# Performance work log

Measured on AMD Instinct MI355X. Metric: run time of the kernel, lower is better.

Reference implementation:

```python
import jax, jax.numpy as jnp
import numpy as np

B, N, G = 32, 262144, 256


def setup_inputs() -> dict:
    key = jax.random.key(0)
    k1, k2, k3 = jax.random.split(key, 3)
    pr = jax.random.normal(k1, (B, N), dtype=jnp.float32)
    inp_means = jax.random.normal(k2, (B, G), dtype=jnp.float32)
    vr = jax.random.randint(k3, (B, N, 1), 0, G, dtype=jnp.int32)
    W = jnp.ones((2,), dtype=jnp.float32)  # hist_weight, ones initializer
    return {"pr": pr, "inp_means": inp_means, "vr": vr, "W": W}


def reference(pr, inp_means, vr, W):
    sg = jax.lax.stop_gradient
    G = inp_means.shape[1]
    v = jnp.squeeze(vr, -1)  # [B, N] int cluster ids (stop_gradient in orig; int anyway)
    p_sg = sg(pr)

    # Per-batch segmented min/max/sum/any over clusters (replaces python loop over g).
    def seg(p, psg, vi):
        mn = jnp.full((G,), jnp.inf, p.dtype).at[vi].min(psg)    # min(where(gidx, pr, inf))
        mx = jnp.full((G,), -jnp.inf, p.dtype).at[vi].max(psg)   # max(where(gidx, pr, -inf))
        sm = jnp.zeros((G,), p.dtype).at[vi].add(p)              # sum(where(gidx, pr, 0))
        any_ = jnp.zeros((G,), bool).at[vi].set(True)            # reduce_any(gidx)
        return mn, mx, sm, any_

    vmins, vmaxs, vsum, vany = jax.vmap(seg)(pr, p_sg, v)  # each [B, G]
    # Original divides sum by cast(any)->1.0 (or 0/0=nan -> 0), i.e. the group SUM.
    vmeans = jnp.where(vany, vsum, jnp.zeros((), pr.dtype))
    vmeans = (inp_means * W[0] + vmeans * W[1]) / (W[0] + W[1])

    no_scale = vmins == vmaxs  # [B, G]
    vmins_g = jnp.take_along_axis(jnp.where(no_scale, 0.0, vmins), v, axis=1)  # [B, N]
    vmaxs_g = jnp.take_along_axis(jnp.where(no_scale, 1.0, vmaxs), v, axis=1)  # [B, N]

    sort_ids = jnp.argsort(vmeans, axis=1)
    orig_ids = jnp.argsort(sort_ids, axis=1)  # inverse permutation
    vs = jnp.take_along_axis(vmeans, sort_ids, axis=1)  # [B, G]
    cd = jnp.concatenate([vs[:, :1], vs, vs[:, -1:] * 2], axis=1)  # [B, G+2]
    # conv1d with kernel ones(2)/c, VALID: out[i] = (cd[i] + cd[i+1]) / c
    f0 = (cd[:, :-2] + cd[:, 1:-1]) / 1.999  # conv(...)[:, :-1]
    f1 = (cd[:, 1:-1] + cd[:, 2:]) / 2.001   # conv(...)[:, 1:]
    f0 = jnp.take_along_axis(
        jnp.where(no_scale, 0.0, jnp.take_along_axis(f0, orig_ids, axis=1)), v, axis=1)
    f1 = jnp.take_along_axis(
        jnp.where(no_scale, 1.0, jnp.take_along_axis(f1, orig_ids, axis=1)), v, axis=1)

    tmp = (sg(pr) - sg(vmins_g)) / sg(vmaxs_g - vmins_g) * (f1 - f0) + f0  # [B, N]
    bad = jnp.isnan(tmp) | (tmp == 0.0)
    s = pr / jnp.where(bad, 1.0, tmp)  # safe denominator (grad-safe)
    scale = jnp.where(bad | jnp.isnan(s) | jnp.isinf(s), 0.0, s)
    return pr * scale
```

## Files before the change

kernel.cpp:

```cpp
#include <hip/hip_runtime.h>
#include <math.h>

#define NB 32
#define NN 262144
#define NG 256
#define NC 64
#define CH (NN/NC)
#define SC (CH/4)
#define CD 64
#define ELD (NN/CD)

__global__ __launch_bounds__(256) void k_count(const int* __restrict__ vr,
                                               unsigned long long* __restrict__ wcnt16,
                                               unsigned* __restrict__ gid32){
  __shared__ unsigned sc[4][NG];
  const int t    = threadIdx.x;
  const int lane = t & 63;
  const int w    = t >> 6;
  sc[0][t] = 0u; sc[1][t] = 0u; sc[2][t] = 0u; sc[3][t] = 0u;
  __syncthreads();

  const int b = blockIdx.x / NC;
  const int c = blockIdx.x % NC;
  const size_t base = (size_t)b*NN + (size_t)c*CH;
  const int4* v4 = (const int4*)(vr + base);

#pragma unroll
  for (int i = 0; i < 4; i++){
    int idx = w*256 + i*64 + lane;
    int4 v = v4[idx];
    atomicAdd(&sc[w][v.x], 1u);
    atomicAdd(&sc[w][v.y], 1u);
    atomicAdd(&sc[w][v.z], 1u);
    atomicAdd(&sc[w][v.w], 1u);
    gid32[(base >> 2) + idx] =
      (unsigned)v.x | ((unsigned)v.y << 8) | ((unsigned)v.z << 16) | ((unsigned)v.w << 24);
  }
  __syncthreads();

  unsigned c0 = sc[0][t], c1 = sc[1][t], c2 = sc[2][t], c3 = sc[3][t];
  const size_t cb = (size_t)b*NC + c;
  wcnt16[cb*NG + t] = (unsigned long long)c0
                    | ((unsigned long long)c1 << 16)
                    | ((unsigned long long)c2 << 32)
                    | ((unsigned long long)c3 << 48);
}

__global__ __launch_bounds__(256) void k_offsets(const unsigned long long* __restrict__ wcnt16,
                                                 unsigned* __restrict__ off,
                                                 unsigned* __restrict__ grpbase,
                                                 unsigned* __restrict__ grplen){
  const int b = blockIdx.x;
  const int g = threadIdx.x;

  unsigned v[NC];
#pragma unroll
  for (int c = 0; c < NC; c++){
    unsigned long long x = wcnt16[(size_t)(b*NC + c)*NG + g];
    unsigned lo = (unsigned)x, hi = (unsigned)(x >> 32);
    v[c] = (lo & 0xFFFFu) + (lo >> 16) + (hi & 0xFFFFu) + (hi >> 16);
  }
  unsigned tot = 0;
#pragma unroll
  for (int c = 0; c < NC; c++) tot += v[c];

  __shared__ unsigned ss[NG];
  ss[g] = tot; __syncthreads();
  for (int d = 1; d < NG; d <<= 1){
    unsigned x = (g >= d) ? ss[g - d] : 0u;
    __syncthreads();
    ss[g] += x;
    __syncthreads();
  }
  unsigned base = ss[g] - tot;

  unsigned run = base;
#pragma unroll
  for (int c = 0; c < NC; c++){
    off[(size_t)(b*NC + c)*NG + g] = run;
    run += v[c];
  }
  grpbase[b*NG + g] = base;
  grplen [b*NG + g] = tot;
}

__global__ __launch_bounds__(256) void k_scatter(const float* __restrict__ pr,
                                                 const unsigned* __restrict__ gid32,
                                                 const unsigned* __restrict__ off,
                                                 const unsigned long long* __restrict__ wcnt16,
                                                 float* __restrict__ sorted){
  __shared__ float vbuf[CH];
  __shared__ unsigned char gbuf[CH];
  __shared__ unsigned wcnt[4][NG];
  __shared__ unsigned bias[NG];
  __shared__ unsigned wsum[4];
  const int t    = threadIdx.x;
  const int lane = t & 63;
  const int w    = t >> 6;
  const int b = blockIdx.x / NC;
  const int c = blockIdx.x % NC;
  const size_t base = (size_t)b*NN + (size_t)c*CH;
  const size_t cb   = (size_t)b*NC + c;

  {
    unsigned long long x = wcnt16[cb*NG + t];
    unsigned offt = off[cb*NG + t];
    unsigned lo = (unsigned)x, hi = (unsigned)(x >> 32);
    unsigned w0 = lo & 0xFFFFu, w1 = lo >> 16, w2 = hi & 0xFFFFu, w3 = hi >> 16;
    unsigned tot = w0 + w1 + w2 + w3;

    unsigned v = tot;
#pragma unroll
    for (int d = 1; d < 64; d <<= 1){
      unsigned y = __shfl_up(v, d, 64);
      if (lane >= d) v += y;
    }
    if (lane == 63) wsum[w] = v;
    __syncthreads();
    unsigned pre = 0;
#pragma unroll
    for (int k = 0; k < 3; k++) if (k < w) pre += wsum[k];
    unsigned lb = pre + v - tot;
    wcnt[0][t] = lb;
    wcnt[1][t] = lb + w0;
    wcnt[2][t] = lb + w0 + w1;
    wcnt[3][t] = lb + w0 + w1 + w2;
    bias[t] = offt - lb;
  }
  __syncthreads();

  {
    const unsigned long long below = (lane == 0) ? 0ull : ((1ull << lane) - 1ull);
    const float*    psrc = pr    + base        + (size_t)w*SC;
    const unsigned* gsrc = gid32 + (base >> 2) + (size_t)w*(SC/4);
    const int shft = (lane & 3) * 8;

    float pv[16]; unsigned pk[16];
#pragma unroll
    for (int s = 0; s < 16; s++){
      pv[s] = psrc[s*64 + lane];
      pk[s] = gsrc[s*16 + (lane >> 2)];
    }
#pragma unroll
    for (int s = 0; s < 16; s++){
      int g = (int)((pk[s] >> shft) & 255u);
      unsigned long long mask = ~0ull;
#pragma unroll
      for (int bit = 0; bit < 8; bit++){
        int bv = (g >> bit) & 1;
        unsigned long long bal = __ballot(bv);
        mask &= bv ? bal : ~bal;
      }
      int rank = __popcll(mask & below);
      unsigned old = wcnt[w][g];
      if (rank == 0) wcnt[w][g] = old + (unsigned)__popcll(mask);
      vbuf[old + (unsigned)rank] = pv[s];
      gbuf[old + (unsigned)rank] = (unsigned char)g;
    }
  }
  __syncthreads();

  {
    float* dst = sorted + (size_t)b*NN;
    const unsigned* gbuf32 = (const unsigned*)gbuf;
#pragma unroll
    for (int k = 0; k < CH/256; k++){
      int p = k*256 + t;
      unsigned packed = gbuf32[p >> 2];
      unsigned g = (packed >> ((p & 3) * 8)) & 255u;
      dst[bias[g] + (unsigned)p] = vbuf[p];
    }
  }
}

__global__ __launch_bounds__(32) void k_sum(const float* __restrict__ sorted,
                                            const unsigned* __restrict__ grpbase,
                                            const unsigned* __restrict__ grplen,
                                            float* __restrict__ gsum,
                                            float* __restrict__ gmn,
                                            float* __restrict__ gmx){
  const int lane = threadIdx.x;
  const int b = blockIdx.x >> 3;
  const int g = ((blockIdx.x & 7) << 5) + lane;

  const unsigned base = grpbase[b*NG + g];
  const unsigned len  = grplen [b*NG + g];
  const float* sp = sorted + (size_t)b*NN + base;

  float s = 0.0f, mn = INFINITY, mx = -INFINITY;

  unsigned head = (4u - ((unsigned)(((size_t)sp) >> 2) & 3u)) & 3u;
  if (head > len) head = len;
  for (unsigned i = 0; i < head; i++){
    float v = sp[i];
    s = __fadd_rn(s, v); mn = fminf(mn, v); mx = fmaxf(mx, v);
  }
  const float4* f4 = (const float4*)(sp + head);
  const unsigned rem   = len - head;
  const unsigned nfull = rem >> 4;

  float4 b0[4], b1[4], b2[4], b3[4], b4[4], b5[4], b6[4], b7[4];
#define LOADV(D, K) { D[0]=f4[(K)*4+0]; D[1]=f4[(K)*4+1]; D[2]=f4[(K)*4+2]; D[3]=f4[(K)*4+3]; }
#define CONS1(V)    { s=__fadd_rn(s,(V)); mn=fminf(mn,(V)); mx=fmaxf(mx,(V)); }
#define CONSV(D)    { _Pragma("unroll") for (int j = 0; j < 4; j++){ float4 q = D[j]; \
                      CONS1(q.x) CONS1(q.y) CONS1(q.z) CONS1(q.w) } }

  if (nfull > 0) LOADV(b0, 0)
  if (nfull > 1) LOADV(b1, 1)
  if (nfull > 2) LOADV(b2, 2)
  if (nfull > 3) LOADV(b3, 3)
  if (nfull > 4) LOADV(b4, 4)
  if (nfull > 5) LOADV(b5, 5)
  if (nfull > 6) LOADV(b6, 6)
  if (nfull > 7) LOADV(b7, 7)
  unsigned k = 0;
  for (; k + 8 <= nfull; k += 8){
    CONSV(b0) if (k +  8 < nfull) LOADV(b0, k +  8)
    CONSV(b1) if (k +  9 < nfull) LOADV(b1, k +  9)
    CONSV(b2) if (k + 10 < nfull) LOADV(b2, k + 10)
    CONSV(b3) if (k + 11 < nfull) LOADV(b3, k + 11)
    CONSV(b4) if (k + 12 < nfull) LOADV(b4, k + 12)
    CONSV(b5) if (k + 13 < nfull) LOADV(b5, k + 13)
    CONSV(b6) if (k + 14 < nfull) LOADV(b6, k + 14)
    CONSV(b7) if (k + 15 < nfull) LOADV(b7, k + 15)
  }
  {
    unsigned r = nfull - k;
    if (r > 0) CONSV(b0)
    if (r > 1) CONSV(b1)
    if (r > 2) CONSV(b2)
    if (r > 3) CONSV(b3)
    if (r > 4) CONSV(b4)
    if (r > 5) CONSV(b5)
    if (r > 6) CONSV(b6)
  }
  for (unsigned i = head + (nfull << 4); i < len; i++){
    float v = sp[i];
    s = __fadd_rn(s, v); mn = fminf(mn, v); mx = fmaxf(mx, v);
  }
#undef LOADV
#undef CONS1
#undef CONSV

  gsum[b*NG + g] = s;
  gmn [b*NG + g] = mn;
  gmx [b*NG + g] = mx;
}

__global__ __launch_bounds__(256) void k_pipeline(const float* __restrict__ gsum,
                                                  const float* __restrict__ gmn,
                                                  const float* __restrict__ gmx,
                                                  const float* __restrict__ inp_means,
                                                  const float* __restrict__ Wv,
                                                  float* __restrict__ params){
  const int b = blockIdx.x;
  const int g = threadIdx.x;
  __shared__ float vm[NG];
  __shared__ float vs[NG];

  const float s   = gsum[b*NG + g];
  const float mnf = gmn [b*NG + g];
  const float mxf = gmx [b*NG + g];
  const float W0 = Wv[0], W1 = Wv[1];
  float mean = __fdiv_rn(__fadd_rn(__fmul_rn(inp_means[b*NG + g], W0),
                                   __fmul_rn(s, W1)),
                         __fadd_rn(W0, W1));
  vm[g] = mean;
  __syncthreads();

  int r = 0;
  for (int j = 0; j < NG; j++){
    float x = vm[j];
    r += (x < mean) || (x == mean && j < g);
  }
  vs[r] = mean;
  __syncthreads();

  float c0 = (r == 0)    ? vs[0]                     : vs[r-1];
  float c1 = vs[r];
  float c2 = (r == NG-1) ? __fmul_rn(vs[NG-1], 2.0f) : vs[r+1];
  float f0 = __fdiv_rn(__fadd_rn(c0, c1), 1.999f);
  float f1 = __fdiv_rn(__fadd_rn(c1, c2), 2.001f);

  bool ns = (mnf == mxf);
  params[(b*4 + 0)*NG + g] = ns ? 0.0f : mnf;
  params[(b*4 + 1)*NG + g] = ns ? 1.0f : __fsub_rn(mxf, mnf);
  params[(b*4 + 2)*NG + g] = ns ? 1.0f : __fsub_rn(f1, f0);
  params[(b*4 + 3)*NG + g] = ns ? 0.0f : f0;
}

static __device__ __forceinline__ float apply_one(float p, unsigned g,
                                                  const float* __restrict__ sp0,
                                                  const float* __restrict__ sp1,
                                                  const float* __restrict__ sp2,
                                                  const float* __restrict__ sp3){
  float t1  = __fsub_rn(p, sp0[g]);
  float t3  = __fdiv_rn(t1, sp1[g]);
  float t5  = __fmul_rn(t3, sp2[g]);
  float tmp = __fadd_rn(t5, sp3[g]);
  bool bad = __builtin_isnan(tmp) || (tmp == 0.0f);
  float s = __fdiv_rn(p, bad ? 1.0f : tmp);
  bool bad2 = bad || __builtin_isnan(s) || __builtin_isinf(s);
  float sc = bad2 ? 0.0f : s;
  return __fmul_rn(p, sc);
}

__global__ __launch_bounds__(256) void k_apply(const float* __restrict__ pr,
                                               const unsigned* __restrict__ gid32,
                                               const float* __restrict__ params,
                                               float* __restrict__ out){
  __shared__ float sp0[NG], sp1[NG], sp2[NG], sp3[NG];
  const int t = threadIdx.x;
  const int b = blockIdx.x / CD;
  const int c = blockIdx.x % CD;

  sp0[t] = params[(b*4 + 0)*NG + t];
  sp1[t] = params[(b*4 + 1)*NG + t];
  sp2[t] = params[(b*4 + 2)*NG + t];
  sp3[t] = params[(b*4 + 3)*NG + t];
  __syncthreads();

  const size_t base = (size_t)b*NN + (size_t)c*ELD;
  const float4* p4 = (const float4*)(pr + base);
  float4* o4 = (float4*)(out + base);

#pragma unroll
  for (int i = 0; i < ELD/1024; i++){
    float4 p = p4[i*256 + t];
    unsigned pk = gid32[(base >> 2) + i*256 + t];
    float4 r;
    r.x = apply_one(p.x,  pk        & 255u, sp0, sp1, sp2, sp3);
    r.y = apply_one(p.y, (pk >>  8) & 255u, sp0, sp1, sp2, sp3);
    r.z = apply_one(p.z, (pk >> 16) & 255u, sp0, sp1, sp2, sp3);
    r.w = apply_one(p.w,  pk >> 24,         sp0, sp1, sp2, sp3);
    o4[i*256 + t] = r;
  }
}

extern "C" void kernel_launch(void* const* d_in, const int* in_sizes, int n_in,
                              void* d_out, int out_size, void* d_ws, size_t ws_size,
                              hipStream_t stream){
  const float* pr        = (const float*)d_in[0];
  const float* inp_means = (const float*)d_in[1];
  const int*   vr        = (const int*)d_in[2];
  const float* W         = (const float*)d_in[3];
  float* out = (float*)d_out;

  char* ws = (char*)d_ws;
  size_t o = 0;
  unsigned long long* wcnt16 = (unsigned long long*)(ws + o); o += (size_t)NB*NC*NG*8;
  unsigned* off     = (unsigned*)(ws + o); o += (size_t)NB*NC*NG*4;
  unsigned* gid32   = (unsigned*)(ws + o); o += (size_t)NB*NN;
  unsigned* grpbase = (unsigned*)(ws + o); o += (size_t)NB*NG*4;
  unsigned* grplen  = (unsigned*)(ws + o); o += (size_t)NB*NG*4;
  float*    gsum    = (float*)   (ws + o); o += (size_t)NB*NG*4;
  float*    gmn     = (float*)   (ws + o); o += (size_t)NB*NG*4;
  float*    gmx     = (float*)   (ws + o); o += (size_t)NB*NG*4;
  float*    params  = (float*)   (ws + o); o += (size_t)NB*NG*16;
  float* sorted = out;

  k_count   <<<NB*NC, 256, 0, stream>>>(vr, wcnt16, gid32);
  k_offsets <<<NB,     NG, 0, stream>>>(wcnt16, off, grpbase, grplen);
  k_scatter <<<NB*NC, 256, 0, stream>>>(pr, gid32, off, wcnt16, sorted);
  k_sum     <<<NB*8,   32, 0, stream>>>(sorted, grpbase, grplen, gsum, gmn, gmx);
  k_pipeline<<<NB,     NG, 0, stream>>>(gsum, gmn, gmx, inp_means, W, params);
  k_apply   <<<NB*CD, 256, 0, stream>>>(pr, gid32, params, out);
}
```

Measured before the change: 173.0 us.

## Precompute per-chunk totals, wave-shuffle scan, vectorize scatter writes and apply loads

k_count now also writes a compact 16-bit per-chunk count so k_offsets reads 2 bytes per entry instead of an 8-byte packed word. k_offsets replaces the shared-memory Hillis-Steele scan with wave-level shuffle scans plus a small cross-wave prefix, which removes many barriers. The scatter writeback processes four elements per thread and issues a single 16-byte store when all four share a group, falling back to scalar stores otherwise. k_apply handles eight elements per thread with wider id loads. These changes cut traffic and barrier overhead at the cost of an extra global write in k_count and divergent branches in the scatter.

```diff
diff --git a/kernel.cpp b/kernel.cpp
--- a/kernel.cpp
+++ b/kernel.cpp
@@ -10,8 +10,11 @@
 #define CD 64
 #define ELD (NN/CD)
 
+struct __attribute__((aligned(4))) f4a { float x, y, z, w; };
+
 __global__ __launch_bounds__(256) void k_count(const int* __restrict__ vr,
                                                unsigned long long* __restrict__ wcnt16,
+                                               unsigned short* __restrict__ cnt16,
                                                unsigned* __restrict__ gid32){
   __shared__ unsigned sc[4][NG];
   const int t    = threadIdx.x;
@@ -44,35 +47,38 @@
                     | ((unsigned long long)c1 << 16)
                     | ((unsigned long long)c2 << 32)
                     | ((unsigned long long)c3 << 48);
-}
-
-__global__ __launch_bounds__(256) void k_offsets(const unsigned long long* __restrict__ wcnt16,
+  cnt16[cb*NG + t] = (unsigned short)(c0 + c1 + c2 + c3);
+}
+
+__global__ __launch_bounds__(256) void k_offsets(const unsigned short* __restrict__ cnt16,
                                                  unsigned* __restrict__ off,
                                                  unsigned* __restrict__ grpbase,
                                                  unsigned* __restrict__ grplen){
   const int b = blockIdx.x;
   const int g = threadIdx.x;
+  const int lane = g & 63;
+  const int w    = g >> 6;
+  __shared__ unsigned wsum[4];
 
   unsigned v[NC];
 #pragma unroll
-  for (int c = 0; c < NC; c++){
-    unsigned long long x = wcnt16[(size_t)(b*NC + c)*NG + g];
-    unsigned lo = (unsigned)x, hi = (unsigned)(x >> 32);
-    v[c] = (lo & 0xFFFFu) + (lo >> 16) + (hi & 0xFFFFu) + (hi >> 16);
-  }
+  for (int c = 0; c < NC; c++) v[c] = cnt16[(size_t)(b*NC + c)*NG + g];
   unsigned tot = 0;
 #pragma unroll
   for (int c = 0; c < NC; c++) tot += v[c];
 
-  __shared__ unsigned ss[NG];
-  ss[g] = tot; __syncthreads();
-  for (int d = 1; d < NG; d <<= 1){
-    unsigned x = (g >= d) ? ss[g - d] : 0u;
-    __syncthreads();
-    ss[g] += x;
-    __syncthreads();
-  }
-  unsigned base = ss[g] - tot;
+  unsigned vscan = tot;
+#pragma unroll
+  for (int d = 1; d < 64; d <<= 1){
+    unsigned y = __shfl_up(vscan, d, 64);
+    if (lane >= d) vscan += y;
+  }
+  if (lane == 63) wsum[w] = vscan;
+  __syncthreads();
+  unsigned pre = 0;
+#pragma unroll
+  for (int k = 0; k < 3; k++) if (k < w) pre += wsum[k];
+  unsigned base = pre + vscan - tot;
 
   unsigned run = base;
 #pragma unroll
@@ -164,11 +170,23 @@
     float* dst = sorted + (size_t)b*NN;
     const unsigned* gbuf32 = (const unsigned*)gbuf;
 #pragma unroll
-    for (int k = 0; k < CH/256; k++){
-      int p = k*256 + t;
-      unsigned packed = gbuf32[p >> 2];
-      unsigned g = (packed >> ((p & 3) * 8)) & 255u;
-      dst[bias[g] + (unsigned)p] = vbuf[p];
+    for (int k = 0; k < CH/1024; k++){
+      int q = k*256 + t;
+      unsigned packed = gbuf32[q];
+      unsigned g0 =  packed        & 255u;
+      unsigned g3 =  packed >> 24;
+      int p = q << 2;
+      float4 v = *(const float4*)&vbuf[p];
+      if (g0 == g3){
+        f4a o; o.x = v.x; o.y = v.y; o.z = v.z; o.w = v.w;
+        *(f4a*)(dst + bias[g0] + (unsigned)p) = o;
+      } else {
+        unsigned g1 = (packed >> 8) & 255u, g2 = (packed >> 16) & 255u;
+        dst[bias[g0] + (unsigned)p    ] = v.x;
+        dst[bias[g1] + (unsigned)p + 1] = v.y;
+        dst[bias[g2] + (unsigned)p + 2] = v.z;
+        dst[bias[g3] + (unsigned)p + 3] = v.w;
+      }
     }
   }
 }
@@ -322,18 +340,26 @@
 
   const size_t base = (size_t)b*NN + (size_t)c*ELD;
   const float4* p4 = (const float4*)(pr + base);
+  const uint2*  g2 = (const uint2*)(gid32 + (base >> 2));
   float4* o4 = (float4*)(out + base);
 
 #pragma unroll
-  for (int i = 0; i < ELD/1024; i++){
-    float4 p = p4[i*256 + t];
-    unsigned pk = gid32[(base >> 2) + i*256 + t];
-    float4 r;
-    r.x = apply_one(p.x,  pk        & 255u, sp0, sp1, sp2, sp3);
-    r.y = apply_one(p.y, (pk >>  8) & 255u, sp0, sp1, sp2, sp3);
-    r.z = apply_one(p.z, (pk >> 16) & 255u, sp0, sp1, sp2, sp3);
-    r.w = apply_one(p.w,  pk >> 24,         sp0, sp1, sp2, sp3);
-    o4[i*256 + t] = r;
+  for (int i = 0; i < ELD/2048; i++){
+    int e8 = i*256 + t;
+    float4 pa = p4[e8*2    ];
+    float4 pb = p4[e8*2 + 1];
+    uint2  pk = g2[e8];
+    float4 ra, rb;
+    ra.x = apply_one(pa.x,  pk.x        & 255u, sp0, sp1, sp2, sp3);
+    ra.y = apply_one(pa.y, (pk.x >>  8) & 255u, sp0, sp1, sp2, sp3);
+    ra.z = apply_one(pa.z, (pk.x >> 16) & 255u, sp0, sp1, sp2, sp3);
+    ra.w = apply_one(pa.w,  pk.x >> 24,         sp0, sp1, sp2, sp3);
+    rb.x = apply_one(pb.x,  pk.y        & 255u, sp0, sp1, sp2, sp3);
+    rb.y = apply_one(pb.y, (pk.y >>  8) & 255u, sp0, sp1, sp2, sp3);
+    rb.z = apply_one(pb.z, (pk.y >> 16) & 255u, sp0, sp1, sp2, sp3);
+    rb.w = apply_one(pb.w,  pk.y >> 24,         sp0, sp1, sp2, sp3);
+    o4[e8*2    ] = ra;
+    o4[e8*2 + 1] = rb;
   }
 }
 
@@ -349,6 +375,7 @@
   char* ws = (char*)d_ws;
   size_t o = 0;
   unsigned long long* wcnt16 = (unsigned long long*)(ws + o); o += (size_t)NB*NC*NG*8;
+  unsigned short* cnt16 = (unsigned short*)(ws + o); o += (size_t)NB*NC*NG*2;
   unsigned* off     = (unsigned*)(ws + o); o += (size_t)NB*NC*NG*4;
   unsigned* gid32   = (unsigned*)(ws + o); o += (size_t)NB*NN;
   unsigned* grpbase = (unsigned*)(ws + o); o += (size_t)NB*NG*4;
@@ -359,10 +386,10 @@
   float*    params  = (float*)   (ws + o); o += (size_t)NB*NG*16;
   float* sorted = out;
 
-  k_count   <<<NB*NC, 256, 0, stream>>>(vr, wcnt16, gid32);
-  k_offsets <<<NB,     NG, 0, stream>>>(wcnt16, off, grpbase, grplen);
+  k_count   <<<NB*NC, 256, 0, stream>>>(vr, wcnt16, cnt16, gid32);
+  k_offsets <<<NB,    256, 0, stream>>>(cnt16, off, grpbase, grplen);
   k_scatter <<<NB*NC, 256, 0, stream>>>(pr, gid32, off, wcnt16, sorted);
   k_sum     <<<NB*8,   32, 0, stream>>>(sorted, grpbase, grplen, gsum, gmn, gmx);
-  k_pipeline<<<NB,     NG, 0, stream>>>(gsum, gmn, gmx, inp_means, W, params);
+  k_pipeline<<<NB,    256, 0, stream>>>(gsum, gmn, gmx, inp_means, W, params);
   k_apply   <<<NB*CD, 256, 0, stream>>>(pr, gid32, params, out);
 }
```

Result: slower. 181.7 us (+5.0%).
